# Kernel optimization log

Measured on AMD Instinct MI355X. Metric: run time of the kernel, lower is better.

Reference implementation:

```python
import jax, jax.numpy as jnp
import numpy as np

B, T0, T1, WIDTH, N, K, H = 1, 512, 1536, 2048, 16, 4, 128
T = T0 + T1
THETA = 1000000.0
ROT = H // 2          # partial_rotary_factor = 0.5 -> rotary dim 64
EPS = 1e-6
NEG = -2.3819763e38


def _rmsnorm(x, scale):
    var = jnp.mean(jnp.square(x.astype(jnp.float32)), axis=-1, keepdims=True)
    normed = x * jnp.reciprocal(jnp.sqrt(var + EPS))
    return (normed * (1.0 + scale)).astype(x.dtype)


def _rope(x, cos, sin):
    # x: [B,T,n,H]; rotate first ROT dims (rotate-half convention), pass-through rest
    xr, xp = x[..., :ROT], x[..., ROT:]
    x1, x2 = jnp.split(xr, 2, axis=-1)
    rot = jnp.concatenate([x1 * cos - x2 * sin, x2 * cos + x1 * sin], axis=-1)
    return jnp.concatenate([rot, xp], axis=-1)


def _stream(x, tm, qg_w, k_w, v_w, qn, kn):
    x = x * tm[..., None].astype(x.dtype)
    qg = jnp.einsum('btd,ndh->btnh', x, qg_w)     # [B,t,N,2H]
    q, gate = jnp.split(qg, 2, axis=-1)
    q = _rmsnorm(q, qn)
    k = _rmsnorm(jnp.einsum('btd,kdh->btkh', x, k_w), kn)
    v = jnp.einsum('btd,kdh->btkh', x, v_w)
    return q, k, v, gate


def setup_inputs():
    key = jax.random.key(0)
    ks = jax.random.split(key, 10)
    f = jnp.float32
    sd = WIDTH ** -0.5
    so = (N * H) ** -0.5
    inp = {}
    inp['x0'] = jax.random.normal(ks[0], (B, T0, WIDTH), f)
    inp['x1'] = jax.random.normal(ks[1], (B, T1, WIDTH), f)
    inp['positions'] = jnp.broadcast_to(jnp.arange(T, dtype=jnp.int32), (B, T))
    inp['attn_mask'] = jnp.broadcast_to(jnp.tril(jnp.ones((T, T), bool)), (B, T, T))
    inp['qg_w0'] = jax.random.normal(ks[2], (N, WIDTH, 2 * H), f) * sd
    inp['k_w0'] = jax.random.normal(ks[3], (K, WIDTH, H), f) * sd
    inp['v_w0'] = jax.random.normal(ks[4], (K, WIDTH, H), f) * sd
    inp['qn0'] = jnp.zeros((H,), f)
    inp['kn0'] = jnp.zeros((H,), f)
    inp['o_w0'] = jax.random.normal(ks[5], (N, H, WIDTH), f) * so
    inp['qg_w1'] = jax.random.normal(ks[6], (N, WIDTH, 2 * H), f) * sd
    inp['k_w1'] = jax.random.normal(ks[7], (K, WIDTH, H), f) * sd
    inp['v_w1'] = jax.random.normal(ks[8], (K, WIDTH, H), f) * sd
    inp['qn1'] = jnp.zeros((H,), f)
    inp['kn1'] = jnp.zeros((H,), f)
    inp['o_w1'] = jax.random.normal(ks[9], (N, H, WIDTH), f) * so
    return inp


def reference(x0, x1, positions, attn_mask,
              qg_w0, k_w0, v_w0, qn0, kn0, o_w0,
              qg_w1, k_w1, v_w1, qn1, kn1, o_w1):
    token_mask = jnp.any(attn_mask, axis=-1)  # [B,T]
    q0, k0, v0, g0 = _stream(x0, token_mask[:, :T0], qg_w0, k_w0, v_w0, qn0, kn0)
    q1, k1, v1, g1 = _stream(x1, token_mask[:, T0:], qg_w1, k_w1, v_w1, qn1, kn1)
    q = jnp.concatenate([q0, q1], axis=1)      # [B,T,N,H]
    k = jnp.concatenate([k0, k1], axis=1)      # [B,T,K,H]
    v = jnp.concatenate([v0, v1], axis=1)
    gate = jnp.concatenate([g0, g1], axis=1)

    half = ROT // 2
    inv_freq = THETA ** (-jnp.arange(half, dtype=jnp.float32) / half)
    ang = positions.astype(jnp.float32)[:, :, None] * inv_freq   # [B,T,half]
    cos = jnp.cos(ang)[:, :, None, :]
    sin = jnp.sin(ang)[:, :, None, :]
    q = _rope(q, cos, sin)
    k = _rope(k, cos, sin)
    q = q * (H ** -0.5)

    cached_k, cached_v = k, v                  # kv_cache is None (prefill)
    rep = N // K
    k = jnp.repeat(k, rep, axis=2)             # [B,T,N,H]
    v = jnp.repeat(v, rep, axis=2)

    mask = attn_mask[:, None, :, :]            # [B,1,T,S]
    logits = jnp.einsum('btnh,bsnh->bnts', q, k, preferred_element_type=jnp.float32)
    masked = jnp.where(mask, logits, NEG)
    probs = jax.nn.softmax(masked, axis=-1).astype(q.dtype)
    probs = probs * jnp.any(mask, axis=-1, keepdims=True).astype(q.dtype)
    enc = jnp.einsum('bnts,bsnh->btnh', probs, v)
    enc = enc * jax.nn.sigmoid(gate).astype(enc.dtype)
    out0 = jnp.einsum('btnh,nhd->btd', enc[:, :T0], o_w0)
    out1 = jnp.einsum('btnh,nhd->btd', enc[:, T0:], o_w1)
    return (out0, out1, cached_k, cached_v)
```

## Files before the change

### kernel.cpp

```cpp
#include <hip/hip_runtime.h>
#include <hip/hip_bf16.h>
#include <cstdint>
#include <cstddef>

#define T0_ 512
#define TT_ 2048
#define WD_ 2048
#define NH_ 16
#define KH_ 4

typedef __attribute__((ext_vector_type(8))) short short8;
typedef __attribute__((ext_vector_type(4))) short short4v;
typedef __attribute__((ext_vector_type(4))) float f32x4;

#define AS1 __attribute__((address_space(1)))
#define AS3 __attribute__((address_space(3)))

__device__ __forceinline__ ushort f2bf(float x) {
  __hip_bfloat16 h = __float2bfloat16(x);
  ushort u; __builtin_memcpy(&u, &h, 2); return u;
}
__device__ __forceinline__ float bf2f(ushort u) {
  __hip_bfloat16 h; __builtin_memcpy(&h, &u, 2);
  return __bfloat162float(h);
}
__device__ __forceinline__ void g2l16(const ushort* g, AS3 ushort* s) {
  __builtin_amdgcn_global_load_lds((const AS1 uint32_t*)g, (AS3 uint32_t*)s, 16, 0, 0);
}

__global__ __launch_bounds__(256) void convert_x(
    const float* __restrict__ x0, const float* __restrict__ x1, ushort* __restrict__ xb)
{
  const int i = blockIdx.x * 256 + threadIdx.x;
  const int e = i * 4;
  const int row = e >> 11, col = e & 2047;
  const float* src = (row < T0_) ? (x0 + (size_t)row * WD_ + col)
                                 : (x1 + (size_t)(row - T0_) * WD_ + col);
  const float4 v = *(const float4*)src;
  ushort4 o; o.x = f2bf(v.x); o.y = f2bf(v.y); o.z = f2bf(v.z); o.w = f2bf(v.w);
  *(ushort4*)(xb + e) = o;
}

__global__ __launch_bounds__(256) void convtrans(
    const float* __restrict__ in, ushort* __restrict__ out, int R, int C)
{
  __shared__ float tile[32][33];
  const int z = blockIdx.z;
  in  += (size_t)z * R * C;
  out += (size_t)z * R * C;
  const int r0 = blockIdx.x * 32, c0 = blockIdx.y * 32;
  const int tx = threadIdx.x & 31, ty = threadIdx.x >> 5;
#pragma unroll
  for (int i = 0; i < 4; ++i)
    tile[ty + 8 * i][tx] = in[(size_t)(r0 + ty + 8 * i) * C + c0 + tx];
  __syncthreads();
#pragma unroll
  for (int i = 0; i < 4; ++i)
    out[(size_t)(c0 + ty + 8 * i) * R + r0 + tx] = f2bf(tile[tx][ty + 8 * i]);
}

__global__ __launch_bounds__(256) void convtrans2(
    const float* __restrict__ s0, const float* __restrict__ s1,
    ushort* __restrict__ d0, ushort* __restrict__ d1, int R, int C, int half)
{
  __shared__ float tile[32][33];
  int z = blockIdx.z;
  const float* in; ushort* out;
  if (z < half) { in = s0 + (size_t)z * R * C; out = d0 + (size_t)z * R * C; }
  else { z -= half; in = s1 + (size_t)z * R * C; out = d1 + (size_t)z * R * C; }
  const int r0 = blockIdx.x * 32, c0 = blockIdx.y * 32;
  const int tx = threadIdx.x & 31, ty = threadIdx.x >> 5;
#pragma unroll
  for (int i = 0; i < 4; ++i)
    tile[ty + 8 * i][tx] = in[(size_t)(r0 + ty + 8 * i) * C + c0 + tx];
  __syncthreads();
#pragma unroll
  for (int i = 0; i < 4; ++i)
    out[(size_t)(c0 + ty + 8 * i) * R + r0 + tx] = f2bf(tile[tx][ty + 8 * i]);
}

__device__ __forceinline__ void gemm_core(
    const ushort* __restrict__ A, const ushort* __restrict__ Bt,
    int row0, int col0, ushort* As, ushort* Bs, f32x4 (&acc)[4][4])
{
  const int tid = threadIdx.x;
  const int w = tid >> 6, l = tid & 63, lq = l >> 4, lm = l & 15;
  const int wr = (w >> 1) * 64, wc = (w & 1) * 64;
  const ushort* Ag = A + (size_t)(row0 + (tid >> 2)) * WD_ + (tid & 3) * 8;
  const ushort* Bg = Bt + (size_t)(col0 + (tid >> 2)) * WD_ + (tid & 3) * 8;
  AS3 ushort* AsW = (AS3 ushort*)As + w * 512;
  AS3 ushort* BsW = (AS3 ushort*)Bs + w * 512;

  for (int k0 = 0; k0 < WD_; k0 += 32) {
    __syncthreads();
    g2l16(Ag + k0, AsW);
    g2l16(Ag + (size_t)64 * WD_ + k0, AsW + 2048);
    g2l16(Bg + k0, BsW);
    g2l16(Bg + (size_t)64 * WD_ + k0, BsW + 2048);
    __syncthreads();
    short8 af[4], bfr[4];
#pragma unroll
    for (int mi = 0; mi < 4; ++mi)
      af[mi] = *(const short8*)&As[(wr + mi * 16 + lm) * 32 + lq * 8];
#pragma unroll
    for (int ni = 0; ni < 4; ++ni)
      bfr[ni] = *(const short8*)&Bs[(wc + ni * 16 + lm) * 32 + lq * 8];
#pragma unroll
    for (int mi = 0; mi < 4; ++mi)
#pragma unroll
      for (int ni = 0; ni < 4; ++ni)
        acc[mi][ni] = __builtin_amdgcn_mfma_f32_16x16x32_bf16(af[mi], bfr[ni], acc[mi][ni], 0, 0, 0);
  }
}

__global__ __launch_bounds__(256) void gemm_proj(
    const ushort* __restrict__ A,
    const ushort* __restrict__ qg0t, const ushort* __restrict__ qg1t,
    const ushort* __restrict__ k0t,  const ushort* __restrict__ k1t,
    const ushort* __restrict__ v0t,  const ushort* __restrict__ v1t,
    ushort* __restrict__ Cqg, float* __restrict__ kc, float* __restrict__ vc)
{
  __shared__ ushort As[4096], Bs[4096];
  const int bx = blockIdx.x;
  const int row0 = blockIdx.y * 128;
  const bool s1 = (row0 >= T0_);
  const ushort* Bt; int col0;
  float* Cf = nullptr; ushort* Cb = nullptr; int ldc;
  if (bx < 32) {
    Bt = s1 ? qg1t : qg0t; col0 = bx * 128; Cb = Cqg; ldc = 4096;
  } else if (bx < 36) {
    Bt = s1 ? k1t : k0t; col0 = (bx - 32) * 128; Cf = kc; ldc = 512;
  } else {
    Bt = s1 ? v1t : v0t; col0 = (bx - 36) * 128; Cf = vc; ldc = 512;
  }
  f32x4 acc[4][4];
#pragma unroll
  for (int mi = 0; mi < 4; ++mi)
#pragma unroll
    for (int ni = 0; ni < 4; ++ni) acc[mi][ni] = (f32x4){0.f, 0.f, 0.f, 0.f};
  gemm_core(A, Bt, row0, col0, As, Bs, acc);
  const int w = threadIdx.x >> 6, l = threadIdx.x & 63, lq = l >> 4, lm = l & 15;
  const int wr = (w >> 1) * 64, wc = (w & 1) * 64;
#pragma unroll
  for (int mi = 0; mi < 4; ++mi)
#pragma unroll
    for (int ni = 0; ni < 4; ++ni)
#pragma unroll
      for (int r = 0; r < 4; ++r) {
        const size_t rr = (size_t)row0 + wr + mi * 16 + lq * 4 + r;
        const size_t cc = (size_t)col0 + wc + ni * 16 + lm;
        if (Cb) Cb[rr * ldc + cc] = f2bf(acc[mi][ni][r]);
        else    Cf[rr * ldc + cc] = acc[mi][ni][r];
      }
}

__global__ __launch_bounds__(256) void gemm_out(
    const ushort* __restrict__ A, const ushort* __restrict__ W0t,
    const ushort* __restrict__ W1t, float* __restrict__ C)
{
  __shared__ ushort As[4096], Bs[4096];
  const int row0 = blockIdx.y * 128, col0 = blockIdx.x * 128;
  const ushort* Bt = (row0 < T0_) ? W0t : W1t;
  f32x4 acc[4][4];
#pragma unroll
  for (int mi = 0; mi < 4; ++mi)
#pragma unroll
    for (int ni = 0; ni < 4; ++ni) acc[mi][ni] = (f32x4){0.f, 0.f, 0.f, 0.f};
  gemm_core(A, Bt, row0, col0, As, Bs, acc);
  const int w = threadIdx.x >> 6, l = threadIdx.x & 63, lq = l >> 4, lm = l & 15;
  const int wr = (w >> 1) * 64, wc = (w & 1) * 64;
#pragma unroll
  for (int mi = 0; mi < 4; ++mi)
#pragma unroll
    for (int ni = 0; ni < 4; ++ni)
#pragma unroll
      for (int r = 0; r < 4; ++r) {
        const size_t rr = (size_t)row0 + wr + mi * 16 + lq * 4 + r;
        const size_t cc = (size_t)col0 + wc + ni * 16 + lm;
        C[rr * 2048 + cc] = acc[mi][ni][r];
      }
}

__global__ __launch_bounds__(256) void postproc(
    ushort* __restrict__ qgb, float* __restrict__ kc, ushort* __restrict__ Kb,
    const int* __restrict__ positions,
    const float* __restrict__ qn0, const float* __restrict__ kn0,
    const float* __restrict__ qn1, const float* __restrict__ kn1)
{
  const int t = blockIdx.x;
  const int w = threadIdx.x >> 6, l = threadIdx.x & 63;
  const float pos = (float)positions[t];
  const bool str1 = (t >= T0_);
  const float* qn = str1 ? qn1 : qn0;
  const float* kn = str1 ? kn1 : kn0;
  const float kfreq = 13.815510557964274f / 32.0f;
  const int h0 = 2 * l, h1 = 2 * l + 1;

  for (int r = w; r < NH_ + KH_; r += 4) {
    const bool isq = (r < NH_);
    float v0, v1; size_t bi; const float* sc;
    if (isq) {
      bi = ((size_t)t * NH_ + r) * 256;
      v0 = bf2f(qgb[bi + h0]); v1 = bf2f(qgb[bi + h1]); sc = qn;
    } else {
      bi = ((size_t)t * KH_ + (r - NH_)) * 128;
      v0 = kc[bi + h0]; v1 = kc[bi + h1]; sc = kn;
    }
    float ss = v0 * v0 + v1 * v1;
#pragma unroll
    for (int off = 32; off > 0; off >>= 1) ss += __shfl_xor(ss, off);
    const float rstd = rsqrtf(ss * (1.0f / 128.0f) + 1e-6f);
    v0 = v0 * rstd * (1.0f + sc[h0]);
    v1 = v1 * rstd * (1.0f + sc[h1]);
    const float p0 = __shfl_xor(v0, 16);
    const float p1 = __shfl_xor(v1, 16);
    if (l < 32) {
      const int i0 = (l < 16) ? h0 : (h0 - 32);
      const float a0 = pos * __expf(-(float)i0 * kfreq);
      const float a1 = pos * __expf(-(float)(i0 + 1) * kfreq);
      const float c0 = cosf(a0), s0 = sinf(a0);
      const float c1 = cosf(a1), s1v = sinf(a1);
      if (l < 16) { v0 = v0 * c0 - p0 * s0; v1 = v1 * c1 - p1 * s1v; }
      else        { v0 = v0 * c0 + p0 * s0; v1 = v1 * c1 + p1 * s1v; }
    }
    if (isq) {
      v0 *= 0.08838834764831843f; v1 *= 0.08838834764831843f;
      qgb[bi + h0] = f2bf(v0); qgb[bi + h1] = f2bf(v1);
    } else {
      kc[bi + h0] = v0; kc[bi + h1] = v1;
      Kb[bi + h0] = f2bf(v0); Kb[bi + h1] = f2bf(v1);
    }
  }
}

__global__ __launch_bounds__(256) void attn(
    const ushort* __restrict__ qgb, const ushort* __restrict__ Kb,
    const ushort* __restrict__ Vt, ushort* __restrict__ encb)
{
  __shared__ ushort Ks[2 * 16384];
  __shared__ ushort Vs[2 * 16384];
  __shared__ ushort Ps[4 * 2048];
  const int tid = threadIdx.x;
  const int w = tid >> 6, l = tid & 63, lq = l >> 4, lm = l & 15;
  const int n = blockIdx.y, kh = n >> 2;

  auto stage = [&](int buf, int s0) {
#pragma unroll
    for (int c = 0; c < 8; ++c) {
      const int row = w * 32 + c * 4 + lq;
      const int ch = lm ^ (row & 15);
      const int dst = buf * 16384 + (w * 32 + c * 4) * 128;
      g2l16(Kb + (size_t)(s0 + row) * 512 + kh * 128 + ch * 8, (AS3 ushort*)Ks + dst);
      g2l16(Vt + (size_t)(kh * 128 + row) * 2048 + s0 + ch * 8, (AS3 ushort*)Vs + dst);
    }
  };

  for (int half = 0; half < 2; ++half) {
    const int qt = half ? (31 - (int)blockIdx.x) : (int)blockIdx.x;
    const int qtb = qt * 64;
    const int nst = qt / 2 + 1;

    short8 aq[4];
    {
      const ushort* qb = qgb + ((size_t)(qtb + w * 16 + lm) * NH_ + n) * 256 + lq * 8;
#pragma unroll
      for (int kk = 0; kk < 4; ++kk) aq[kk] = *(const short8*)(qb + kk * 32);
    }
    f32x4 acc[8];
#pragma unroll
    for (int i = 0; i < 8; ++i) acc[i] = (f32x4){0.f, 0.f, 0.f, 0.f};
    float mq = -3.0e38f, lsum = 0.0f;

    __syncthreads();
    stage(0, 0);

    for (int st = 0; st < nst; ++st) {
      const int buf = st & 1;
      const int s0 = st * 128;
      __syncthreads();
      if (st + 1 < nst) stage(buf ^ 1, s0 + 128);
      const ushort* Kt = Ks + buf * 16384;
      const ushort* Vb = Vs + buf * 16384;

      f32x4 sa[8];
#pragma unroll
      for (int mi = 0; mi < 8; ++mi) sa[mi] = (f32x4){0.f, 0.f, 0.f, 0.f};
#pragma unroll
      for (int kk = 0; kk < 4; ++kk)
#pragma unroll
        for (int mi = 0; mi < 8; ++mi) {
          const short8 ak = *(const short8*)&Kt[(mi * 16 + lm) * 128 + ((kk * 4 + lq) ^ lm) * 8];
          sa[mi] = __builtin_amdgcn_mfma_f32_16x16x32_bf16(ak, aq[kk], sa[mi], 0, 0, 0);
        }
      if (s0 + 127 > qtb) {
        const int qg_ = qtb + w * 16 + lm;
#pragma unroll
        for (int mi = 0; mi < 8; ++mi)
#pragma unroll
          for (int r = 0; r < 4; ++r)
            if (s0 + mi * 16 + lq * 4 + r > qg_) sa[mi][r] = -3.0e38f;
      }
      float mx = sa[0][0];
#pragma unroll
      for (int mi = 0; mi < 8; ++mi)
#pragma unroll
        for (int r = 0; r < 4; ++r) mx = fmaxf(mx, sa[mi][r]);
      mx = fmaxf(mx, __shfl_xor(mx, 16));
      mx = fmaxf(mx, __shfl_xor(mx, 32));
      const float mn = fmaxf(mq, mx);
      const float alpha = __expf(mq - mn);
      mq = mn;
      float sl = 0.0f;
#pragma unroll
      for (int mi = 0; mi < 8; ++mi)
#pragma unroll
        for (int r = 0; r < 4; ++r) {
          const float p = __expf(sa[mi][r] - mn);
          sa[mi][r] = p; sl += p;
        }
      sl += __shfl_xor(sl, 16);
      sl += __shfl_xor(sl, 32);
      lsum = lsum * alpha + sl;

#pragma unroll
      for (int mi = 0; mi < 8; ++mi) {
        short4v pw;
#pragma unroll
        for (int r = 0; r < 4; ++r) pw[r] = (short)f2bf(sa[mi][r]);
        *(short4v*)&Ps[w * 2048 + lm * 128 + (((mi * 4 + lq)) ^ lm) * 4] = pw;
      }
      float aP[4];
#pragma unroll
      for (int r = 0; r < 4; ++r) aP[r] = __shfl(alpha, lq * 4 + r);
#pragma unroll
      for (int hi = 0; hi < 8; ++hi) {
        f32x4 a = acc[hi];
#pragma unroll
        for (int r = 0; r < 4; ++r) a[r] *= aP[r];
        acc[hi] = a;
      }
#pragma unroll
      for (int mi2 = 0; mi2 < 4; ++mi2) {
        const short4v pa = *(const short4v*)&Ps[w * 2048 + lm * 128 + ((mi2 * 8 + lq * 2 + 0) ^ lm) * 4];
        const short4v pb = *(const short4v*)&Ps[w * 2048 + lm * 128 + ((mi2 * 8 + lq * 2 + 1) ^ lm) * 4];
        const short8 ap = __builtin_shufflevector(pa, pb, 0, 1, 2, 3, 4, 5, 6, 7);
#pragma unroll
        for (int hi = 0; hi < 8; ++hi) {
          const short8 bv = *(const short8*)&Vb[(hi * 16 + lm) * 128 + ((mi2 * 4 + lq) ^ lm) * 8];
          acc[hi] = __builtin_amdgcn_mfma_f32_16x16x32_bf16(ap, bv, acc[hi], 0, 0, 0);
        }
      }
    }
    const float linv = 1.0f / lsum;
    float lP[4];
#pragma unroll
    for (int r = 0; r < 4; ++r) lP[r] = __shfl(linv, lq * 4 + r);
#pragma unroll
    for (int hi = 0; hi < 8; ++hi)
#pragma unroll
      for (int r = 0; r < 4; ++r) {
        const int t = qtb + w * 16 + lq * 4 + r;
        const int h = hi * 16 + lm;
        const float g = bf2f(qgb[((size_t)t * NH_ + n) * 256 + 128 + h]);
        const float o = acc[hi][r] * lP[r] * (1.0f / (1.0f + __expf(-g)));
        encb[((size_t)t * NH_ + n) * 128 + h] = f2bf(o);
      }
  }
}

extern "C" void kernel_launch(void* const* d_in, const int* in_sizes, int n_in,
                              void* d_out, int out_size, void* d_ws, size_t ws_size,
                              hipStream_t stream)
{
  (void)in_sizes; (void)n_in; (void)out_size; (void)ws_size;
  const float* x0    = (const float*)d_in[0];
  const float* x1    = (const float*)d_in[1];
  const int*   pos   = (const int*)d_in[2];
  const float* qg_w0 = (const float*)d_in[4];
  const float* k_w0  = (const float*)d_in[5];
  const float* v_w0  = (const float*)d_in[6];
  const float* qn0   = (const float*)d_in[7];
  const float* kn0   = (const float*)d_in[8];
  const float* o_w0  = (const float*)d_in[9];
  const float* qg_w1 = (const float*)d_in[10];
  const float* k_w1  = (const float*)d_in[11];
  const float* v_w1  = (const float*)d_in[12];
  const float* qn1   = (const float*)d_in[13];
  const float* kn1   = (const float*)d_in[14];
  const float* o_w1  = (const float*)d_in[15];

  float* out    = (float*)d_out;
  float* kcache = out + (size_t)TT_ * WD_;
  float* vcache = kcache + (size_t)TT_ * KH_ * 128;
  ushort* qsc = (ushort*)d_out;

  ushort* wbuf = (ushort*)d_ws;
  ushort* xb   = wbuf + 8388608;
  ushort* qgb  = xb + 4194304;
  ushort* encb = qgb + 8388608;
  ushort* Kbuf = xb;
  ushort* Vtb  = xb + 1048576;
  ushort* k0t = encb, *k1t = encb + 1048576, *v0t = encb + 2097152, *v1t = encb + 3145728;

  convert_x<<<4096, 256, 0, stream>>>(x0, x1, xb);

  convtrans2<<<dim3(64, 8, 32), 256, 0, stream>>>(qg_w0, qg_w1, qsc, wbuf, WD_, 256, 16);
  convtrans2<<<dim3(64, 4, 8), 256, 0, stream>>>(k_w0, k_w1, k0t, k1t, WD_, 128, 4);
  convtrans2<<<dim3(64, 4, 8), 256, 0, stream>>>(v_w0, v_w1, v0t, v1t, WD_, 128, 4);

  gemm_proj<<<dim3(40, 16), 256, 0, stream>>>(xb, qsc, wbuf, k0t, k1t, v0t, v1t,
                                              qgb, kcache, vcache);

  postproc<<<2048, 256, 0, stream>>>(qgb, kcache, Kbuf, pos, qn0, kn0, qn1, kn1);
  convtrans<<<dim3(64, 16, 1), 256, 0, stream>>>(vcache, Vtb, TT_, 512);

  attn<<<dim3(16, 16), 256, 0, stream>>>(qgb, Kbuf, Vtb, encb);

  convtrans2<<<dim3(64, 64, 2), 256, 0, stream>>>(o_w0, o_w1, wbuf, wbuf + 4194304, WD_, WD_, 1);
  gemm_out<<<dim3(16, 16), 256, 0, stream>>>(encb, wbuf, wbuf + 4194304, out);
}
```

Baseline: 399.3 us.

## Split attention into one q-tile per block and vectorize weight transposes

```diff
diff --git a/kernel.cpp b/kernel.cpp
--- a/kernel.cpp
+++ b/kernel.cpp
@@ -41,42 +41,34 @@
   *(ushort4*)(xb + e) = o;
 }
 
-__global__ __launch_bounds__(256) void convtrans(
-    const float* __restrict__ in, ushort* __restrict__ out, int R, int C)
-{
-  __shared__ float tile[32][33];
+struct P4 { const float* s[4]; ushort* d[4]; };
+
+__global__ __launch_bounds__(256) void wtrans4(P4 p, int C, int slabs)
+{
+  __shared__ float tile[64][65];
   const int z = blockIdx.z;
-  in  += (size_t)z * R * C;
-  out += (size_t)z * R * C;
-  const int r0 = blockIdx.x * 32, c0 = blockIdx.y * 32;
-  const int tx = threadIdx.x & 31, ty = threadIdx.x >> 5;
-#pragma unroll
-  for (int i = 0; i < 4; ++i)
-    tile[ty + 8 * i][tx] = in[(size_t)(r0 + ty + 8 * i) * C + c0 + tx];
+  const int tz = z / slabs, sz = z % slabs;
+  const float* in = p.s[tz] + (size_t)sz * 2048 * C;
+  ushort* out = p.d[tz] + (size_t)sz * 2048 * C;
+  const int r0 = blockIdx.x * 64, c0 = blockIdx.y * 64;
+  const int t = threadIdx.x;
+  const int lr = t >> 4, lc = (t & 15) * 4;
+#pragma unroll
+  for (int pp = 0; pp < 4; ++pp) {
+    const float4 v = *(const float4*)(in + (size_t)(r0 + lr + 16 * pp) * C + c0 + lc);
+    tile[lr + 16 * pp][lc + 0] = v.x; tile[lr + 16 * pp][lc + 1] = v.y;
+    tile[lr + 16 * pp][lc + 2] = v.z; tile[lr + 16 * pp][lc + 3] = v.w;
+  }
   __syncthreads();
-#pragma unroll
-  for (int i = 0; i < 4; ++i)
-    out[(size_t)(c0 + ty + 8 * i) * R + r0 + tx] = f2bf(tile[tx][ty + 8 * i]);
-}
-
-__global__ __launch_bounds__(256) void convtrans2(
-    const float* __restrict__ s0, const float* __restrict__ s1,
-    ushort* __restrict__ d0, ushort* __restrict__ d1, int R, int C, int half)
-{
-  __shared__ float tile[32][33];
-  int z = blockIdx.z;
-  const float* in; ushort* out;
-  if (z < half) { in = s0 + (size_t)z * R * C; out = d0 + (size_t)z * R * C; }
-  else { z -= half; in = s1 + (size_t)z * R * C; out = d1 + (size_t)z * R * C; }
-  const int r0 = blockIdx.x * 32, c0 = blockIdx.y * 32;
-  const int tx = threadIdx.x & 31, ty = threadIdx.x >> 5;
-#pragma unroll
-  for (int i = 0; i < 4; ++i)
-    tile[ty + 8 * i][tx] = in[(size_t)(r0 + ty + 8 * i) * C + c0 + tx];
-  __syncthreads();
-#pragma unroll
-  for (int i = 0; i < 4; ++i)
-    out[(size_t)(c0 + ty + 8 * i) * R + r0 + tx] = f2bf(tile[tx][ty + 8 * i]);
+  const int oc = t >> 4, rj = (t & 15) * 4;
+#pragma unroll
+  for (int pp = 0; pp < 4; ++pp) {
+    const int orow = oc + 16 * pp;
+    ushort4 o;
+    o.x = f2bf(tile[rj + 0][orow]); o.y = f2bf(tile[rj + 1][orow]);
+    o.z = f2bf(tile[rj + 2][orow]); o.w = f2bf(tile[rj + 3][orow]);
+    *(ushort4*)(out + (size_t)(c0 + orow) * 2048 + r0 + rj) = o;
+  }
 }
 
 __device__ __forceinline__ void gemm_core(
@@ -237,135 +229,127 @@
     const ushort* __restrict__ qgb, const ushort* __restrict__ Kb,
     const ushort* __restrict__ Vt, ushort* __restrict__ encb)
 {
-  __shared__ ushort Ks[2 * 16384];
-  __shared__ ushort Vs[2 * 16384];
+  __shared__ ushort Ks[16384];
+  __shared__ ushort Vs[16384];
   __shared__ ushort Ps[4 * 2048];
   const int tid = threadIdx.x;
   const int w = tid >> 6, l = tid & 63, lq = l >> 4, lm = l & 15;
+  const int qt = (int)gridDim.x - 1 - (int)blockIdx.x;
   const int n = blockIdx.y, kh = n >> 2;
-
-  auto stage = [&](int buf, int s0) {
+  const int qtb = qt * 64;
+  const int nst = qt / 2 + 1;
+
+  auto stage = [&](int s0) {
 #pragma unroll
     for (int c = 0; c < 8; ++c) {
       const int row = w * 32 + c * 4 + lq;
       const int ch = lm ^ (row & 15);
-      const int dst = buf * 16384 + (w * 32 + c * 4) * 128;
+      const int dst = (w * 32 + c * 4) * 128;
       g2l16(Kb + (size_t)(s0 + row) * 512 + kh * 128 + ch * 8, (AS3 ushort*)Ks + dst);
       g2l16(Vt + (size_t)(kh * 128 + row) * 2048 + s0 + ch * 8, (AS3 ushort*)Vs + dst);
     }
   };
 
-  for (int half = 0; half < 2; ++half) {
-    const int qt = half ? (31 - (int)blockIdx.x) : (int)blockIdx.x;
-    const int qtb = qt * 64;
-    const int nst = qt / 2 + 1;
-
-    short8 aq[4];
-    {
-      const ushort* qb = qgb + ((size_t)(qtb + w * 16 + lm) * NH_ + n) * 256 + lq * 8;
-#pragma unroll
-      for (int kk = 0; kk < 4; ++kk) aq[kk] = *(const short8*)(qb + kk * 32);
-    }
-    f32x4 acc[8];
-#pragma unroll
-    for (int i = 0; i < 8; ++i) acc[i] = (f32x4){0.f, 0.f, 0.f, 0.f};
-    float mq = -3.0e38f, lsum = 0.0f;
-
+  short8 aq[4];
+  {
+    const ushort* qb = qgb + ((size_t)(qtb + w * 16 + lm) * NH_ + n) * 256 + lq * 8;
+#pragma unroll
+    for (int kk = 0; kk < 4; ++kk) aq[kk] = *(const short8*)(qb + kk * 32);
+  }
+  f32x4 acc[8];
+#pragma unroll
+  for (int i = 0; i < 8; ++i) acc[i] = (f32x4){0.f, 0.f, 0.f, 0.f};
+  float mq = -3.0e38f, lsum = 0.0f;
+
+  for (int st = 0; st < nst; ++st) {
+    const int s0 = st * 128;
+    stage(s0);
     __syncthreads();
-    stage(0, 0);
-
-    for (int st = 0; st < nst; ++st) {
-      const int buf = st & 1;
-      const int s0 = st * 128;
-      __syncthreads();
-      if (st + 1 < nst) stage(buf ^ 1, s0 + 128);
-      const ushort* Kt = Ks + buf * 16384;
-      const ushort* Vb = Vs + buf * 16384;
-
-      f32x4 sa[8];
-#pragma unroll
-      for (int mi = 0; mi < 8; ++mi) sa[mi] = (f32x4){0.f, 0.f, 0.f, 0.f};
-#pragma unroll
-      for (int kk = 0; kk < 4; ++kk)
-#pragma unroll
-        for (int mi = 0; mi < 8; ++mi) {
-          const short8 ak = *(const short8*)&Kt[(mi * 16 + lm) * 128 + ((kk * 4 + lq) ^ lm) * 8];
-          sa[mi] = __builtin_amdgcn_mfma_f32_16x16x32_bf16(ak, aq[kk], sa[mi], 0, 0, 0);
-        }
-      if (s0 + 127 > qtb) {
-        const int qg_ = qtb + w * 16 + lm;
-#pragma unroll
-        for (int mi = 0; mi < 8; ++mi)
-#pragma unroll
-          for (int r = 0; r < 4; ++r)
-            if (s0 + mi * 16 + lq * 4 + r > qg_) sa[mi][r] = -3.0e38f;
+
+    f32x4 sa[8];
+#pragma unroll
+    for (int mi = 0; mi < 8; ++mi) sa[mi] = (f32x4){0.f, 0.f, 0.f, 0.f};
+#pragma unroll
+    for (int kk = 0; kk < 4; ++kk)
+#pragma unroll
+      for (int mi = 0; mi < 8; ++mi) {
+        const short8 ak = *(const short8*)&Ks[(mi * 16 + lm) * 128 + ((kk * 4 + lq) ^ lm) * 8];
+        sa[mi] = __builtin_amdgcn_mfma_f32_16x16x32_bf16(ak, aq[kk], sa[mi], 0, 0, 0);
       }
-      float mx = sa[0][0];
+    if (s0 + 127 > qtb) {
+      const int qg_ = qtb + w * 16 + lm;
 #pragma unroll
       for (int mi = 0; mi < 8; ++mi)
 #pragma unroll
-        for (int r = 0; r < 4; ++r) mx = fmaxf(mx, sa[mi][r]);
-      mx = fmaxf(mx, __shfl_xor(mx, 16));
-      mx = fmaxf(mx, __shfl_xor(mx, 32));
-      const float mn = fmaxf(mq, mx);
-      const float alpha = __expf(mq - mn);
-      mq = mn;
-      float sl = 0.0f;
-#pragma unroll
-      for (int mi = 0; mi < 8; ++mi)
-#pragma unroll
-        for (int r = 0; r < 4; ++r) {
-          const float p = __expf(sa[mi][r] - mn);
-          sa[mi][r] = p; sl += p;
-        }
-      sl += __shfl_xor(sl, 16);
-      sl += __shfl_xor(sl, 32);
-      lsum = lsum * alpha + sl;
-
-#pragma unroll
-      for (int mi = 0; mi < 8; ++mi) {
-        short4v pw;
-#pragma unroll
-        for (int r = 0; r < 4; ++r) pw[r] = (short)f2bf(sa[mi][r]);
-        *(short4v*)&Ps[w * 2048 + lm * 128 + (((mi * 4 + lq)) ^ lm) * 4] = pw;
+        for (int r = 0; r < 4; ++r)
+          if (s0 + mi * 16 + lq * 4 + r > qg_) sa[mi][r] = -3.0e38f;
+    }
+    float mx = sa[0][0];
+#pragma unroll
+    for (int mi = 0; mi < 8; ++mi)
+#pragma unroll
+      for (int r = 0; r < 4; ++r) mx = fmaxf(mx, sa[mi][r]);
+    mx = fmaxf(mx, __shfl_xor(mx, 16));
+    mx = fmaxf(mx, __shfl_xor(mx, 32));
+    const float mn = fmaxf(mq, mx);
+    const float alpha = __expf(mq - mn);
+    mq = mn;
+    float sl = 0.0f;
+#pragma unroll
+    for (int mi = 0; mi < 8; ++mi)
+#pragma unroll
+      for (int r = 0; r < 4; ++r) {
+        const float p = __expf(sa[mi][r] - mn);
+        sa[mi][r] = p; sl += p;
       }
-      float aP[4];
-#pragma unroll
-      for (int r = 0; r < 4; ++r) aP[r] = __shfl(alpha, lq * 4 + r);
+    sl += __shfl_xor(sl, 16);
+    sl += __shfl_xor(sl, 32);
+    lsum = lsum * alpha + sl;
+
+#pragma unroll
+    for (int mi = 0; mi < 8; ++mi) {
+      short4v pw;
+#pragma unroll
+      for (int r = 0; r < 4; ++r) pw[r] = (short)f2bf(sa[mi][r]);
+      *(short4v*)&Ps[w * 2048 + lm * 128 + (((mi * 4 + lq)) ^ lm) * 4] = pw;
+    }
+    float aP[4];
+#pragma unroll
+    for (int r = 0; r < 4; ++r) aP[r] = __shfl(alpha, lq * 4 + r);
+#pragma unroll
+    for (int hi = 0; hi < 8; ++hi) {
+      f32x4 a = acc[hi];
+#pragma unroll
+      for (int r = 0; r < 4; ++r) a[r] *= aP[r];
+      acc[hi] = a;
+    }
+#pragma unroll
+    for (int mi2 = 0; mi2 < 4; ++mi2) {
+      const short4v pa = *(const short4v*)&Ps[w * 2048 + lm * 128 + ((mi2 * 8 + lq * 2 + 0) ^ lm) * 4];
+      const short4v pb = *(const short4v*)&Ps[w * 2048 + lm * 128 + ((mi2 * 8 + lq * 2 + 1) ^ lm) * 4];
+      const short8 ap = __builtin_shufflevector(pa, pb, 0, 1, 2, 3, 4, 5, 6, 7);
 #pragma unroll
       for (int hi = 0; hi < 8; ++hi) {
-        f32x4 a = acc[hi];
-#pragma unroll
-        for (int r = 0; r < 4; ++r) a[r] *= aP[r];
-        acc[hi] = a;
+        const short8 bv = *(const short8*)&Vs[(hi * 16 + lm) * 128 + ((mi2 * 4 + lq) ^ lm) * 8];
+        acc[hi] = __builtin_amdgcn_mfma_f32_16x16x32_bf16(ap, bv, acc[hi], 0, 0, 0);
       }
-#pragma unroll
-      for (int mi2 = 0; mi2 < 4; ++mi2) {
-        const short4v pa = *(const short4v*)&Ps[w * 2048 + lm * 128 + ((mi2 * 8 + lq * 2 + 0) ^ lm) * 4];
-        const short4v pb = *(const short4v*)&Ps[w * 2048 + lm * 128 + ((mi2 * 8 + lq * 2 + 1) ^ lm) * 4];
-        const short8 ap = __builtin_shufflevector(pa, pb, 0, 1, 2, 3, 4, 5, 6, 7);
-#pragma unroll
-        for (int hi = 0; hi < 8; ++hi) {
-          const short8 bv = *(const short8*)&Vb[(hi * 16 + lm) * 128 + ((mi2 * 4 + lq) ^ lm) * 8];
-          acc[hi] = __builtin_amdgcn_mfma_f32_16x16x32_bf16(ap, bv, acc[hi], 0, 0, 0);
-        }
-      }
-    }
-    const float linv = 1.0f / lsum;
-    float lP[4];
-#pragma unroll
-    for (int r = 0; r < 4; ++r) lP[r] = __shfl(linv, lq * 4 + r);
-#pragma unroll
-    for (int hi = 0; hi < 8; ++hi)
-#pragma unroll
-      for (int r = 0; r < 4; ++r) {
-        const int t = qtb + w * 16 + lq * 4 + r;
-        const int h = hi * 16 + lm;
-        const float g = bf2f(qgb[((size_t)t * NH_ + n) * 256 + 128 + h]);
-        const float o = acc[hi][r] * lP[r] * (1.0f / (1.0f + __expf(-g)));
-        encb[((size_t)t * NH_ + n) * 128 + h] = f2bf(o);
-      }
-  }
+    }
+    __syncthreads();
+  }
+  const float linv = 1.0f / lsum;
+  float lP[4];
+#pragma unroll
+  for (int r = 0; r < 4; ++r) lP[r] = __shfl(linv, lq * 4 + r);
+#pragma unroll
+  for (int hi = 0; hi < 8; ++hi)
+#pragma unroll
+    for (int r = 0; r < 4; ++r) {
+      const int t = qtb + w * 16 + lq * 4 + r;
+      const int h = hi * 16 + lm;
+      const float g = bf2f(qgb[((size_t)t * NH_ + n) * 256 + 128 + h]);
+      const float o = acc[hi][r] * lP[r] * (1.0f / (1.0f + __expf(-g)));
+      encb[((size_t)t * NH_ + n) * 128 + h] = f2bf(o);
+    }
 }
 
 extern "C" void kernel_launch(void* const* d_in, const int* in_sizes, int n_in,
@@ -404,18 +388,21 @@
 
   convert_x<<<4096, 256, 0, stream>>>(x0, x1, xb);
 
-  convtrans2<<<dim3(64, 8, 32), 256, 0, stream>>>(qg_w0, qg_w1, qsc, wbuf, WD_, 256, 16);
-  convtrans2<<<dim3(64, 4, 8), 256, 0, stream>>>(k_w0, k_w1, k0t, k1t, WD_, 128, 4);
-  convtrans2<<<dim3(64, 4, 8), 256, 0, stream>>>(v_w0, v_w1, v0t, v1t, WD_, 128, 4);
+  P4 jq = {{qg_w0, qg_w1, nullptr, nullptr}, {qsc, wbuf, nullptr, nullptr}};
+  wtrans4<<<dim3(32, 4, 32), 256, 0, stream>>>(jq, 256, 16);
+  P4 jkv = {{k_w0, k_w1, v_w0, v_w1}, {k0t, k1t, v0t, v1t}};
+  wtrans4<<<dim3(32, 2, 16), 256, 0, stream>>>(jkv, 128, 4);
 
   gemm_proj<<<dim3(40, 16), 256, 0, stream>>>(xb, qsc, wbuf, k0t, k1t, v0t, v1t,
                                               qgb, kcache, vcache);
 
   postproc<<<2048, 256, 0, stream>>>(qgb, kcache, Kbuf, pos, qn0, kn0, qn1, kn1);
-  convtrans<<<dim3(64, 16, 1), 256, 0, stream>>>(vcache, Vtb, TT_, 512);
-
-  attn<<<dim3(16, 16), 256, 0, stream>>>(qgb, Kbuf, Vtb, encb);
-
-  convtrans2<<<dim3(64, 64, 2), 256, 0, stream>>>(o_w0, o_w1, wbuf, wbuf + 4194304, WD_, WD_, 1);
+  P4 jv = {{vcache, nullptr, nullptr, nullptr}, {Vtb, nullptr, nullptr, nullptr}};
+  wtrans4<<<dim3(32, 8, 1), 256, 0, stream>>>(jv, 512, 1);
+
+  attn<<<dim3(32, 16), 256, 0, stream>>>(qgb, Kbuf, Vtb, encb);
+
+  P4 jo = {{o_w0, o_w1, nullptr, nullptr}, {wbuf, wbuf + 4194304, nullptr, nullptr}};
+  wtrans4<<<dim3(32, 32, 2), 256, 0, stream>>>(jo, 2048, 1);
   gemm_out<<<dim3(16, 16), 256, 0, stream>>>(encb, wbuf, wbuf + 4194304, out);
 }
```

New measurement: 405.0 us. No clear change (+1.4%).
